# Kernel optimization log

Hardware: AMD Instinct MI355X
Metric: run time of the kernel (lower is better)

The kernel has to match this reference:

```python
import jax, jax.numpy as jnp
import numpy as np

N_NODES = 100000
N_EDGES = 1600000
IN_CH = 128
HID = 64
OUT_CH = 16
N_GRAPHS = 512
NEG_SLOPE = 0.2


def setup_inputs() -> dict:
    key = jax.random.key(0)
    ks = jax.random.split(key, 24)
    x = jax.random.normal(ks[0], (N_NODES, IN_CH), dtype=jnp.float32)
    edge_index = jax.random.randint(ks[1], (2, N_EDGES), 0, N_NODES, dtype=jnp.int64)
    batch = jnp.sort(jax.random.randint(ks[2], (N_NODES,), 0, N_GRAPHS, dtype=jnp.int64))
    s = 0.05
    p = {
        'W_l1': jax.random.normal(ks[3], (IN_CH, HID)) * s,
        'b_l1': jnp.zeros((HID,), jnp.float32),
        'W_r1': jax.random.normal(ks[4], (IN_CH, HID)) * s,
        'b_r1': jnp.zeros((HID,), jnp.float32),
        'att1': jax.random.normal(ks[5], (HID,)) * s,
        'bias1': jnp.zeros((HID,), jnp.float32),
        'W_l2': jax.random.normal(ks[6], (HID, HID)) * s,
        'b_l2': jnp.zeros((HID,), jnp.float32),
        'W_r2': jax.random.normal(ks[7], (HID, HID)) * s,
        'b_r2': jnp.zeros((HID,), jnp.float32),
        'att2': jax.random.normal(ks[8], (HID,)) * s,
        'bias2': jnp.zeros((HID,), jnp.float32),
        'W_fc1': jax.random.normal(ks[9], (HID, HID)) * s,
        'b_fc1': jnp.zeros((HID,), jnp.float32),
        'gamma': jnp.ones((HID,), jnp.float32),
        'beta': jnp.zeros((HID,), jnp.float32),
        'W_fc2': jax.random.normal(ks[10], (HID, OUT_CH)) * s,
        'b_fc2': jnp.zeros((OUT_CH,), jnp.float32),
    }
    return dict(x=x, edge_index=edge_index, batch=batch, **p)


def _gatv2_layer(x, src, dst, Wl, bl, Wr, br, att, bias):
    # GATv2Conv (heads=1): x_l = lin_l(x), x_r = lin_r(x)
    xl = x @ Wl + bl              # [N, H] source transform
    xr = x @ Wr + br              # [N, H] target transform
    # per-edge score: att . LeakyReLU(x_l[j] + x_r[i])
    h = xl[src] + xr[dst]         # [E, H]
    h = jnp.where(h >= 0, h, NEG_SLOPE * h)
    e = h @ att                   # [E]
    # scatter-softmax over incoming edges of each target node
    m = jax.ops.segment_max(e, dst, num_segments=N_NODES)
    a = jnp.exp(e - m[dst])
    z = jax.ops.segment_sum(a, dst, num_segments=N_NODES)
    alpha = a / z[dst]            # every node has a self-loop -> z > 0
    out = jax.ops.segment_sum(alpha[:, None] * xl[src], dst, num_segments=N_NODES)
    return out + bias


def reference(x, edge_index, batch, W_l1, b_l1, W_r1, b_r1, att1, bias1,
              W_l2, b_l2, W_r2, b_r2, att2, bias2,
              W_fc1, b_fc1, gamma, beta, W_fc2, b_fc2):
    loop = jnp.arange(N_NODES, dtype=edge_index.dtype)
    src = jnp.concatenate([edge_index[0], loop])  # add_self_loops=True
    dst = jnp.concatenate([edge_index[1], loop])
    h = _gatv2_layer(x, src, dst, W_l1, b_l1, W_r1, b_r1, att1, bias1)
    h = jax.nn.relu(h)
    h = _gatv2_layer(h, src, dst, W_l2, b_l2, W_r2, b_r2, att2, bias2)
    # global mean pool over graphs
    sums = jax.ops.segment_sum(h, batch, num_segments=N_GRAPHS)
    cnt = jax.ops.segment_sum(jnp.ones((N_NODES,), h.dtype), batch, num_segments=N_GRAPHS)
    g = sums / jnp.clip(cnt, 1.0)[:, None]        # [G, H]
    # MLP head: Linear -> BatchNorm1d (training-mode batch stats) -> ReLU -> Linear
    y = g @ W_fc1 + b_fc1
    mu = jnp.mean(y, axis=0)
    var = jnp.var(y, axis=0)
    y = gamma * (y - mu) * jax.lax.rsqrt(var + 1e-5) + beta
    y = jax.nn.relu(y)
    y = y @ W_fc2 + b_fc2
    return jax.nn.log_softmax(y, axis=1)
```

## Files before the change

### kernel.cpp

```cpp
#include <hip/hip_runtime.h>

#define N_NODES 100000
#define N_EDGES 1600000
#define IN_CH 128
#define HID 64
#define OUT_CH 16
#define N_GRAPHS 512
#define NEG_SLOPE 0.2f

#define MAX_DEG 64

#define GEMM1_BLOCKS ((N_NODES + 127) / 128)
#define DEG_EPT 8
#define DEG_BLOCKS ((N_EDGES + 256 * DEG_EPT - 1) / (256 * DEG_EPT))
#define FUSED_BLOCKS (GEMM1_BLOCKS + DEG_BLOCKS)

#define NEG_BIG (-1e30f)
#define LDSP 132

__device__ __forceinline__ unsigned int f2bf_pack(float lo, float hi) {
  unsigned int ul = __float_as_uint(lo);
  unsigned int uh = __float_as_uint(hi);
  ul = (ul + 0x7FFFu + ((ul >> 16) & 1u)) >> 16;
  uh = (uh + 0x7FFFu + ((uh >> 16) & 1u)) >> 16;
  return ul | (uh << 16);
}
__device__ __forceinline__ float bf2f(unsigned short b) {
  return __uint_as_float(((unsigned int)b) << 16);
}


__global__ __launch_bounds__(256) void k_fused_gemm1_scatter(
    const float* __restrict__ x,
    const float* __restrict__ Wl, const float* __restrict__ bl,
    const float* __restrict__ Wr, const float* __restrict__ br,
    unsigned short* __restrict__ xlb, unsigned short* __restrict__ xrb,
    const int* __restrict__ src, const int* __restrict__ dst,
    int* __restrict__ deg, int* __restrict__ adjP) {
  constexpr int K = IN_CH;
  constexpr int KC = 16;
  constexpr int NCH = K / KC;
  __shared__ float xs[KC][LDSP];
  __shared__ float ws[KC][LDSP];

  int b = blockIdx.x;
  if (b & 1) {
    int db = b >> 1;
    int base = (db * 256 + threadIdx.x) * DEG_EPT;
    if (base + DEG_EPT <= N_EDGES) {
      int4 d4a = *(const int4*)&dst[base];
      int4 d4b = *(const int4*)&dst[base + 4];
      int4 s4a = *(const int4*)&src[base];
      int4 s4b = *(const int4*)&src[base + 4];
      int sl;
      sl = atomicAdd(&deg[d4a.x], 1); if (sl < MAX_DEG) adjP[d4a.x * MAX_DEG + sl] = s4a.x;
      sl = atomicAdd(&deg[d4a.y], 1); if (sl < MAX_DEG) adjP[d4a.y * MAX_DEG + sl] = s4a.y;
      sl = atomicAdd(&deg[d4a.z], 1); if (sl < MAX_DEG) adjP[d4a.z * MAX_DEG + sl] = s4a.z;
      sl = atomicAdd(&deg[d4a.w], 1); if (sl < MAX_DEG) adjP[d4a.w * MAX_DEG + sl] = s4a.w;
      sl = atomicAdd(&deg[d4b.x], 1); if (sl < MAX_DEG) adjP[d4b.x * MAX_DEG + sl] = s4b.x;
      sl = atomicAdd(&deg[d4b.y], 1); if (sl < MAX_DEG) adjP[d4b.y * MAX_DEG + sl] = s4b.y;
      sl = atomicAdd(&deg[d4b.z], 1); if (sl < MAX_DEG) adjP[d4b.z * MAX_DEG + sl] = s4b.z;
      sl = atomicAdd(&deg[d4b.w], 1); if (sl < MAX_DEG) adjP[d4b.w * MAX_DEG + sl] = s4b.w;
    } else {
      for (int e = base; e < N_EDGES; e++) {
        int d = dst[e];
        int sl = atomicAdd(&deg[d], 1);
        if (sl < MAX_DEG) adjP[d * MAX_DEG + sl] = src[e];
      }
    }
    return;
  }

  int tid = threadIdx.x;
  int tx = tid & 15;
  int ty = tid >> 4;
  int nb = (b >> 1) * 128;

  float acc[8][8];
  #pragma unroll
  for (int i = 0; i < 8; i++)
    #pragma unroll
    for (int j = 0; j < 8; j++) acc[i][j] = 0.f;

  for (int c = 0; c < NCH; c++) {
    int kc = c * KC;
    if (c) __syncthreads();
    #pragma unroll
    for (int j = 0; j < 2; j++) {
      int idx = tid + 256 * j;
      int node = idx >> 2, q = idx & 3;
      int gn = nb + node;
      float4 v = make_float4(0.f, 0.f, 0.f, 0.f);
      if (gn < N_NODES) v = *(const float4*)&x[(size_t)gn * K + kc + q * 4];
      xs[q * 4 + 0][node] = v.x;
      xs[q * 4 + 1][node] = v.y;
      xs[q * 4 + 2][node] = v.z;
      xs[q * 4 + 3][node] = v.w;
    }
    #pragma unroll
    for (int j = 0; j < 2; j++) {
      int idx = tid + 256 * j;
      int k = idx >> 5, cc = idx & 31;
      float4 v;
      if (cc < 16) v = *(const float4*)&Wl[(size_t)(kc + k) * 64 + cc * 4];
      else         v = *(const float4*)&Wr[(size_t)(kc + k) * 64 + (cc - 16) * 4];
      *(float4*)&ws[k][cc * 4] = v;
    }
    __syncthreads();

    #pragma unroll 4
    for (int k = 0; k < KC; k++) {
      float4 a0 = *(const float4*)&xs[k][ty * 8];
      float4 a1 = *(const float4*)&xs[k][ty * 8 + 4];
      float4 b0 = *(const float4*)&ws[k][tx * 8];
      float4 b1 = *(const float4*)&ws[k][tx * 8 + 4];
      float av[8] = {a0.x, a0.y, a0.z, a0.w, a1.x, a1.y, a1.z, a1.w};
      float bv[8] = {b0.x, b0.y, b0.z, b0.w, b1.x, b1.y, b1.z, b1.w};
      #pragma unroll
      for (int i = 0; i < 8; i++)
        #pragma unroll
        for (int j = 0; j < 8; j++)
          acc[i][j] = fmaf(av[i], bv[j], acc[i][j]);
    }
  }

  int f0 = tx * 8;
  float bb[8];
  #pragma unroll
  for (int j = 0; j < 8; j++)
    bb[j] = (f0 < 64) ? bl[f0 + j] : br[f0 - 64 + j];
  unsigned short* outp = (f0 < 64) ? xlb : xrb;
  int fo = (f0 < 64) ? f0 : f0 - 64;
  #pragma unroll
  for (int i = 0; i < 8; i++) {
    int node = nb + ty * 8 + i;
    if (node < N_NODES) {
      int4 o;
      o.x = (int)f2bf_pack(acc[i][0] + bb[0], acc[i][1] + bb[1]);
      o.y = (int)f2bf_pack(acc[i][2] + bb[2], acc[i][3] + bb[3]);
      o.z = (int)f2bf_pack(acc[i][4] + bb[4], acc[i][5] + bb[5]);
      o.w = (int)f2bf_pack(acc[i][6] + bb[6], acc[i][7] + bb[7]);
      *(int4*)&outp[(size_t)node * 64 + fo] = o;
    }
  }
}


template <int K>
__global__ __launch_bounds__(256) void k_dual_gemm(
    const float* __restrict__ x,
    const float* __restrict__ Wl, const float* __restrict__ bl,
    const float* __restrict__ Wr, const float* __restrict__ br,
    unsigned short* __restrict__ xlb, unsigned short* __restrict__ xrb) {
  constexpr int KC = 32;
  constexpr int NCH = K / KC;
  __shared__ float xs[KC][LDSP];
  __shared__ float ws[KC][LDSP];

  int tid = threadIdx.x;
  int tx = tid & 15;
  int ty = tid >> 4;
  int nb = blockIdx.x * 128;

  float acc[8][8];
  #pragma unroll
  for (int i = 0; i < 8; i++)
    #pragma unroll
    for (int j = 0; j < 8; j++) acc[i][j] = 0.f;

  for (int c = 0; c < NCH; c++) {
    int kc = c * KC;
    if (c) __syncthreads();
    #pragma unroll
    for (int j = 0; j < 4; j++) {
      int idx = tid + 256 * j;
      int node = idx >> 3, q = idx & 7;
      int gn = nb + node;
      float4 v = make_float4(0.f, 0.f, 0.f, 0.f);
      if (gn < N_NODES) v = *(const float4*)&x[(size_t)gn * K + kc + q * 4];
      xs[q * 4 + 0][node] = v.x;
      xs[q * 4 + 1][node] = v.y;
      xs[q * 4 + 2][node] = v.z;
      xs[q * 4 + 3][node] = v.w;
    }
    #pragma unroll
    for (int j = 0; j < 4; j++) {
      int idx = tid + 256 * j;
      int k = idx >> 5, cc = idx & 31;
      float4 v;
      if (cc < 16) v = *(const float4*)&Wl[(size_t)(kc + k) * 64 + cc * 4];
      else         v = *(const float4*)&Wr[(size_t)(kc + k) * 64 + (cc - 16) * 4];
      *(float4*)&ws[k][cc * 4] = v;
    }
    __syncthreads();

    #pragma unroll 4
    for (int k = 0; k < KC; k++) {
      float4 a0 = *(const float4*)&xs[k][ty * 8];
      float4 a1 = *(const float4*)&xs[k][ty * 8 + 4];
      float4 b0 = *(const float4*)&ws[k][tx * 8];
      float4 b1 = *(const float4*)&ws[k][tx * 8 + 4];
      float av[8] = {a0.x, a0.y, a0.z, a0.w, a1.x, a1.y, a1.z, a1.w};
      float bv[8] = {b0.x, b0.y, b0.z, b0.w, b1.x, b1.y, b1.z, b1.w};
      #pragma unroll
      for (int i = 0; i < 8; i++)
        #pragma unroll
        for (int j = 0; j < 8; j++)
          acc[i][j] = fmaf(av[i], bv[j], acc[i][j]);
    }
  }

  int f0 = tx * 8;
  float bb[8];
  #pragma unroll
  for (int j = 0; j < 8; j++)
    bb[j] = (f0 < 64) ? bl[f0 + j] : br[f0 - 64 + j];
  unsigned short* outp = (f0 < 64) ? xlb : xrb;
  int fo = (f0 < 64) ? f0 : f0 - 64;
  #pragma unroll
  for (int i = 0; i < 8; i++) {
    int node = nb + ty * 8 + i;
    if (node < N_NODES) {
      int4 o;
      o.x = (int)f2bf_pack(acc[i][0] + bb[0], acc[i][1] + bb[1]);
      o.y = (int)f2bf_pack(acc[i][2] + bb[2], acc[i][3] + bb[3]);
      o.z = (int)f2bf_pack(acc[i][4] + bb[4], acc[i][5] + bb[5]);
      o.w = (int)f2bf_pack(acc[i][6] + bb[6], acc[i][7] + bb[7]);
      *(int4*)&outp[(size_t)node * 64 + fo] = o;
    }
  }
}


__global__ __launch_bounds__(256) void k_gat(
    const unsigned short* __restrict__ xlb, const unsigned short* __restrict__ xrb,
    const float* __restrict__ att, const float* __restrict__ bias,
    const int* __restrict__ deg, const int* __restrict__ adjP,
    float* __restrict__ out, int do_relu) {
  int wid = (blockIdx.x * 256 + threadIdx.x) >> 6;
  int lane = threadIdx.x & 63;
  if (wid >= N_NODES) return;
  int fg = lane & 15;
  int sub = lane >> 4;

  int degv = deg[wid];
  degv = (degv < MAX_DEG) ? degv : MAX_DEG;
  int L = degv + 1;

  int eidx = wid;
  if (lane < degv) eidx = adjP[(size_t)wid * MAX_DEG + lane];

  ushort4 xrr = *(const ushort4*)&xrb[(size_t)wid * 64 + fg * 4];
  float4 xr4;
  xr4.x = bf2f(xrr.x); xr4.y = bf2f(xrr.y); xr4.z = bf2f(xrr.z); xr4.w = bf2f(xrr.w);
  float4 att4 = *(const float4*)&att[fg * 4];

  float m = NEG_BIG, z = 0.f;
  float4 acc = make_float4(0.f, 0.f, 0.f, 0.f);

  for (int p0 = 0; p0 < L; p0 += 8) {
    int q0 = p0 + sub * 2;
    int q1 = q0 + 1;
    bool act0 = (q0 < L);
    bool act1 = (q1 < L);
    int idx0 = q0 - 1;
    int idx1 = q1 - 1;
    int sj0 = __shfl(eidx, idx0 & 63, 64);
    int sj1 = __shfl(eidx, idx1 & 63, 64);
    int j0 = (q0 == 0) ? wid : sj0;
    int j1 = sj1;
    ushort4 raw0 = make_ushort4(0, 0, 0, 0);
    ushort4 raw1 = make_ushort4(0, 0, 0, 0);
    if (act0) raw0 = *(const ushort4*)&xlb[(size_t)j0 * 64 + fg * 4];
    if (act1) raw1 = *(const ushort4*)&xlb[(size_t)j1 * 64 + fg * 4];
    float4 v0, v1;
    v0.x = bf2f(raw0.x); v0.y = bf2f(raw0.y); v0.z = bf2f(raw0.z); v0.w = bf2f(raw0.w);
    v1.x = bf2f(raw1.x); v1.y = bf2f(raw1.y); v1.z = bf2f(raw1.z); v1.w = bf2f(raw1.w);

    float ax, ay, az, aw;
    ax = v0.x + xr4.x; ax = (ax >= 0.f) ? ax : NEG_SLOPE * ax;
    ay = v0.y + xr4.y; ay = (ay >= 0.f) ? ay : NEG_SLOPE * ay;
    az = v0.z + xr4.z; az = (az >= 0.f) ? az : NEG_SLOPE * az;
    aw = v0.w + xr4.w; aw = (aw >= 0.f) ? aw : NEG_SLOPE * aw;
    float s0 = fmaf(ax, att4.x, fmaf(ay, att4.y, fmaf(az, att4.z, aw * att4.w)));
    ax = v1.x + xr4.x; ax = (ax >= 0.f) ? ax : NEG_SLOPE * ax;
    ay = v1.y + xr4.y; ay = (ay >= 0.f) ? ay : NEG_SLOPE * ay;
    az = v1.z + xr4.z; az = (az >= 0.f) ? az : NEG_SLOPE * az;
    aw = v1.w + xr4.w; aw = (aw >= 0.f) ? aw : NEG_SLOPE * aw;
    float s1 = fmaf(ax, att4.x, fmaf(ay, att4.y, fmaf(az, att4.z, aw * att4.w)));
    #pragma unroll
    for (int o = 1; o <= 8; o <<= 1) {
      s0 += __shfl_xor(s0, o, 64);
      s1 += __shfl_xor(s1, o, 64);
    }
    float e0 = act0 ? s0 : NEG_BIG;
    float e1 = act1 ? s1 : NEG_BIG;

    float nm = fmaxf(m, fmaxf(e0, e1));
    float sc = __expf(m - nm);
    float w0 = __expf(e0 - nm);
    float w1 = __expf(e1 - nm);
    z = fmaf(z, sc, w0 + w1);
    acc.x = fmaf(acc.x, sc, fmaf(w0, v0.x, w1 * v1.x));
    acc.y = fmaf(acc.y, sc, fmaf(w0, v0.y, w1 * v1.y));
    acc.z = fmaf(acc.z, sc, fmaf(w0, v0.z, w1 * v1.z));
    acc.w = fmaf(acc.w, sc, fmaf(w0, v0.w, w1 * v1.w));
    m = nm;
  }

  #pragma unroll
  for (int o = 16; o <= 32; o <<= 1) {
    float m2 = __shfl_xor(m, o, 64);
    float z2 = __shfl_xor(z, o, 64);
    float a0 = __shfl_xor(acc.x, o, 64);
    float a1 = __shfl_xor(acc.y, o, 64);
    float a2 = __shfl_xor(acc.z, o, 64);
    float a3 = __shfl_xor(acc.w, o, 64);
    float nm = fmaxf(m, m2);
    float s1 = __expf(m - nm);
    float s2 = __expf(m2 - nm);
    z = z * s1 + z2 * s2;
    acc.x = acc.x * s1 + a0 * s2;
    acc.y = acc.y * s1 + a1 * s2;
    acc.z = acc.z * s1 + a2 * s2;
    acc.w = acc.w * s1 + a3 * s2;
    m = nm;
  }

  if (sub == 0) {
    float4 b4 = *(const float4*)&bias[fg * 4];
    float inv = 1.f / z;
    float4 r;
    r.x = acc.x * inv + b4.x;
    r.y = acc.y * inv + b4.y;
    r.z = acc.z * inv + b4.z;
    r.w = acc.w * inv + b4.w;
    if (do_relu) {
      r.x = fmaxf(r.x, 0.f); r.y = fmaxf(r.y, 0.f);
      r.z = fmaxf(r.z, 0.f); r.w = fmaxf(r.w, 0.f);
    }
    *(float4*)&out[(size_t)wid * 64 + fg * 4] = r;
  }
}


__device__ __forceinline__ int lower_bound_batch(const int* __restrict__ b, int key) {
  int lo = 0, hi = N_NODES;
  while (lo < hi) {
    int mid = (lo + hi) >> 1;
    if (b[mid] < key) lo = mid + 1; else hi = mid;
  }
  return lo;
}

__global__ void k_pool(const float* __restrict__ h, const int* __restrict__ batch,
                       float* __restrict__ gmean) {
  __shared__ int s_range[2];
  __shared__ float red[256];
  int g = blockIdx.x, t = threadIdx.x;
  if (t == 0) s_range[0] = lower_bound_batch(batch, g);
  if (t == 1) s_range[1] = lower_bound_batch(batch, g + 1);
  __syncthreads();
  int lo = s_range[0], hi = s_range[1];
  int f = t & 63, sub = t >> 6;
  float acc = 0.f;
  for (int n = lo + sub; n < hi; n += 4) acc += h[n * 64 + f];
  red[t] = acc;
  __syncthreads();
  if (sub == 0) {
    float s = red[f] + red[64 + f] + red[128 + f] + red[192 + f];
    int cnt = hi - lo;
    if (cnt < 1) cnt = 1;
    gmean[g * 64 + f] = s / (float)cnt;
  }
}


__global__ void k_head1(const float* __restrict__ gmean, const float* __restrict__ W,
                        const float* __restrict__ b, float* __restrict__ y) {
  int idx = blockIdx.x * 256 + threadIdx.x;
  if (idx >= N_GRAPHS * 64) return;
  int gi = idx >> 6, f = idx & 63;
  float acc = b[f];
  #pragma unroll 8
  for (int k = 0; k < 64; k++) acc = fmaf(gmean[gi * 64 + k], W[k * 64 + f], acc);
  y[idx] = acc;
}

__global__ void k_bnstats(const float* __restrict__ y, float* __restrict__ mu,
                          float* __restrict__ rstd) {
  __shared__ float red_s[256], red_ss[256];
  int t = threadIdx.x;
  int f = t & 63, grp = t >> 6;
  float s = 0.f, ss = 0.f;
  for (int g = grp; g < N_GRAPHS; g += 4) {
    float v = y[g * 64 + f];
    s += v;
    ss += v * v;
  }
  red_s[t] = s;
  red_ss[t] = ss;
  __syncthreads();
  if (t < 64) {
    s = red_s[t] + red_s[64 + t] + red_s[128 + t] + red_s[192 + t];
    ss = red_ss[t] + red_ss[64 + t] + red_ss[128 + t] + red_ss[192 + t];
    float m = s / (float)N_GRAPHS;
    float var = ss / (float)N_GRAPHS - m * m;
    mu[t] = m;
    rstd[t] = rsqrtf(var + 1e-5f);
  }
}

__global__ void k_head2(const float* __restrict__ y, const float* __restrict__ gamma,
                        const float* __restrict__ beta, const float* __restrict__ mu,
                        const float* __restrict__ rstd, const float* __restrict__ W2,
                        const float* __restrict__ b2, float* __restrict__ out) {
  int idx = blockIdx.x * 256 + threadIdx.x;
  if (idx >= N_GRAPHS * OUT_CH) return;
  int gi = idx >> 4, o = idx & 15;
  float acc = b2[o];
  #pragma unroll
  for (int k = 0; k < 64; k++) {
    float v = y[gi * 64 + k];
    v = gamma[k] * (v - mu[k]) * rstd[k] + beta[k];
    v = fmaxf(v, 0.f);
    acc = fmaf(v, W2[k * OUT_CH + o], acc);
  }
  float mx = acc;
  #pragma unroll
  for (int w = 8; w > 0; w >>= 1) mx = fmaxf(mx, __shfl_xor(mx, w, 16));
  float ex = __expf(acc - mx);
  float s = ex;
  #pragma unroll
  for (int w = 8; w > 0; w >>= 1) s += __shfl_xor(s, w, 16);
  out[idx] = acc - mx - __logf(s);
}


extern "C" void kernel_launch(void* const* d_in, const int* in_sizes, int n_in,
                              void* d_out, int out_size, void* d_ws, size_t ws_size,
                              hipStream_t stream) {
  const float* x      = (const float*)d_in[0];
  const int*   edge   = (const int*)d_in[1];
  const int*   batch  = (const int*)d_in[2];
  const float* W_l1   = (const float*)d_in[3];
  const float* b_l1   = (const float*)d_in[4];
  const float* W_r1   = (const float*)d_in[5];
  const float* b_r1   = (const float*)d_in[6];
  const float* att1   = (const float*)d_in[7];
  const float* bias1  = (const float*)d_in[8];
  const float* W_l2   = (const float*)d_in[9];
  const float* b_l2   = (const float*)d_in[10];
  const float* W_r2   = (const float*)d_in[11];
  const float* b_r2   = (const float*)d_in[12];
  const float* att2   = (const float*)d_in[13];
  const float* bias2  = (const float*)d_in[14];
  const float* W_fc1  = (const float*)d_in[15];
  const float* b_fc1  = (const float*)d_in[16];
  const float* gamma  = (const float*)d_in[17];
  const float* beta   = (const float*)d_in[18];
  const float* W_fc2  = (const float*)d_in[19];
  const float* b_fc2  = (const float*)d_in[20];

  const int* src = edge;
  const int* dst = edge + N_EDGES;

  char* ws = (char*)d_ws;
  size_t off = 0;
  auto alloc = [&](size_t bytes) -> void* {
    off = (off + 255) & ~(size_t)255;
    void* p = ws + off;
    off += bytes;
    return p;
  };
  int* deg      = (int*)alloc((size_t)N_NODES * 4);
  int* adjP     = (int*)alloc((size_t)N_NODES * MAX_DEG * 4);
  unsigned short* xlb = (unsigned short*)alloc((size_t)N_NODES * HID * 2);
  unsigned short* xrb = (unsigned short*)alloc((size_t)N_NODES * HID * 2);
  float* h      = (float*)alloc((size_t)N_NODES * HID * 4);
  float* gmean  = (float*)alloc((size_t)N_GRAPHS * HID * 4);
  float* y      = (float*)alloc((size_t)N_GRAPHS * HID * 4);
  float* mu     = (float*)alloc(64 * 4);
  float* rstd   = (float*)alloc(64 * 4);

  hipMemsetAsync(deg, 0, (size_t)N_NODES * 4, stream);

  k_fused_gemm1_scatter<<<FUSED_BLOCKS, 256, 0, stream>>>(
      x, W_l1, b_l1, W_r1, b_r1, xlb, xrb, src, dst, deg, adjP);

  k_gat<<<(N_NODES + 3) / 4, 256, 0, stream>>>(xlb, xrb, att1, bias1, deg, adjP, h, 1);
  k_dual_gemm<HID><<<(N_NODES + 127) / 128, 256, 0, stream>>>(h, W_l2, b_l2, W_r2, b_r2, xlb, xrb);
  k_gat<<<(N_NODES + 3) / 4, 256, 0, stream>>>(xlb, xrb, att2, bias2, deg, adjP, h, 0);

  k_pool<<<N_GRAPHS, 256, 0, stream>>>(h, batch, gmean);
  k_head1<<<(N_GRAPHS * 64 + 255) / 256, 256, 0, stream>>>(gmean, W_fc1, b_fc1, y);
  k_bnstats<<<1, 256, 0, stream>>>(y, mu, rstd);
  k_head2<<<(N_GRAPHS * OUT_CH + 255) / 256, 256, 0, stream>>>(y, gamma, beta, mu, rstd,
                                                               W_fc2, b_fc2, (float*)d_out);
}
```

Baseline: 436.4 us.

## Fuse layer-2 dual linear transform into first GAT aggregation epilogue

Result: slower. 469.8 us (+7.7%).

```diff
diff --git a/kernel.cpp b/kernel.cpp
--- a/kernel.cpp
+++ b/kernel.cpp
@@ -24,6 +24,11 @@
   ul = (ul + 0x7FFFu + ((ul >> 16) & 1u)) >> 16;
   uh = (uh + 0x7FFFu + ((uh >> 16) & 1u)) >> 16;
   return ul | (uh << 16);
+}
+__device__ __forceinline__ unsigned short f2bf(float v) {
+  unsigned int u = __float_as_uint(v);
+  u = (u + 0x7FFFu + ((u >> 16) & 1u)) >> 16;
+  return (unsigned short)u;
 }
 __device__ __forceinline__ float bf2f(unsigned short b) {
   return __uint_as_float(((unsigned int)b) << 16);
@@ -146,97 +151,14 @@
 }
 
 
-template <int K>
-__global__ __launch_bounds__(256) void k_dual_gemm(
-    const float* __restrict__ x,
-    const float* __restrict__ Wl, const float* __restrict__ bl,
-    const float* __restrict__ Wr, const float* __restrict__ br,
-    unsigned short* __restrict__ xlb, unsigned short* __restrict__ xrb) {
-  constexpr int KC = 32;
-  constexpr int NCH = K / KC;
-  __shared__ float xs[KC][LDSP];
-  __shared__ float ws[KC][LDSP];
-
-  int tid = threadIdx.x;
-  int tx = tid & 15;
-  int ty = tid >> 4;
-  int nb = blockIdx.x * 128;
-
-  float acc[8][8];
-  #pragma unroll
-  for (int i = 0; i < 8; i++)
-    #pragma unroll
-    for (int j = 0; j < 8; j++) acc[i][j] = 0.f;
-
-  for (int c = 0; c < NCH; c++) {
-    int kc = c * KC;
-    if (c) __syncthreads();
-    #pragma unroll
-    for (int j = 0; j < 4; j++) {
-      int idx = tid + 256 * j;
-      int node = idx >> 3, q = idx & 7;
-      int gn = nb + node;
-      float4 v = make_float4(0.f, 0.f, 0.f, 0.f);
-      if (gn < N_NODES) v = *(const float4*)&x[(size_t)gn * K + kc + q * 4];
-      xs[q * 4 + 0][node] = v.x;
-      xs[q * 4 + 1][node] = v.y;
-      xs[q * 4 + 2][node] = v.z;
-      xs[q * 4 + 3][node] = v.w;
-    }
-    #pragma unroll
-    for (int j = 0; j < 4; j++) {
-      int idx = tid + 256 * j;
-      int k = idx >> 5, cc = idx & 31;
-      float4 v;
-      if (cc < 16) v = *(const float4*)&Wl[(size_t)(kc + k) * 64 + cc * 4];
-      else         v = *(const float4*)&Wr[(size_t)(kc + k) * 64 + (cc - 16) * 4];
-      *(float4*)&ws[k][cc * 4] = v;
-    }
-    __syncthreads();
-
-    #pragma unroll 4
-    for (int k = 0; k < KC; k++) {
-      float4 a0 = *(const float4*)&xs[k][ty * 8];
-      float4 a1 = *(const float4*)&xs[k][ty * 8 + 4];
-      float4 b0 = *(const float4*)&ws[k][tx * 8];
-      float4 b1 = *(const float4*)&ws[k][tx * 8 + 4];
-      float av[8] = {a0.x, a0.y, a0.z, a0.w, a1.x, a1.y, a1.z, a1.w};
-      float bv[8] = {b0.x, b0.y, b0.z, b0.w, b1.x, b1.y, b1.z, b1.w};
-      #pragma unroll
-      for (int i = 0; i < 8; i++)
-        #pragma unroll
-        for (int j = 0; j < 8; j++)
-          acc[i][j] = fmaf(av[i], bv[j], acc[i][j]);
-    }
-  }
-
-  int f0 = tx * 8;
-  float bb[8];
-  #pragma unroll
-  for (int j = 0; j < 8; j++)
-    bb[j] = (f0 < 64) ? bl[f0 + j] : br[f0 - 64 + j];
-  unsigned short* outp = (f0 < 64) ? xlb : xrb;
-  int fo = (f0 < 64) ? f0 : f0 - 64;
-  #pragma unroll
-  for (int i = 0; i < 8; i++) {
-    int node = nb + ty * 8 + i;
-    if (node < N_NODES) {
-      int4 o;
-      o.x = (int)f2bf_pack(acc[i][0] + bb[0], acc[i][1] + bb[1]);
-      o.y = (int)f2bf_pack(acc[i][2] + bb[2], acc[i][3] + bb[3]);
-      o.z = (int)f2bf_pack(acc[i][4] + bb[4], acc[i][5] + bb[5]);
-      o.w = (int)f2bf_pack(acc[i][6] + bb[6], acc[i][7] + bb[7]);
-      *(int4*)&outp[(size_t)node * 64 + fo] = o;
-    }
-  }
-}
-
-
 __global__ __launch_bounds__(256) void k_gat(
     const unsigned short* __restrict__ xlb, const unsigned short* __restrict__ xrb,
     const float* __restrict__ att, const float* __restrict__ bias,
     const int* __restrict__ deg, const int* __restrict__ adjP,
-    float* __restrict__ out, int do_relu) {
+    const float* __restrict__ Wl2, const float* __restrict__ bl2,
+    const float* __restrict__ Wr2, const float* __restrict__ br2,
+    unsigned short* __restrict__ xlb_out, unsigned short* __restrict__ xrb_out,
+    float* __restrict__ hout, int mode) {
   int wid = (blockIdx.x * 256 + threadIdx.x) >> 6;
   int lane = threadIdx.x & 63;
   if (wid >= N_NODES) return;
@@ -327,19 +249,32 @@
     m = nm;
   }
 
-  if (sub == 0) {
-    float4 b4 = *(const float4*)&bias[fg * 4];
-    float inv = 1.f / z;
-    float4 r;
-    r.x = acc.x * inv + b4.x;
-    r.y = acc.y * inv + b4.y;
-    r.z = acc.z * inv + b4.z;
-    r.w = acc.w * inv + b4.w;
-    if (do_relu) {
-      r.x = fmaxf(r.x, 0.f); r.y = fmaxf(r.y, 0.f);
-      r.z = fmaxf(r.z, 0.f); r.w = fmaxf(r.w, 0.f);
-    }
-    *(float4*)&out[(size_t)wid * 64 + fg * 4] = r;
+  float inv = 1.f / z;
+  float4 b4 = *(const float4*)&bias[fg * 4];
+  float4 r;
+  r.x = acc.x * inv + b4.x;
+  r.y = acc.y * inv + b4.y;
+  r.z = acc.z * inv + b4.z;
+  r.w = acc.w * inv + b4.w;
+
+  if (mode) {
+    r.x = fmaxf(r.x, 0.f); r.y = fmaxf(r.y, 0.f);
+    r.z = fmaxf(r.z, 0.f); r.w = fmaxf(r.w, 0.f);
+    float y0 = 0.f, y1 = 0.f;
+    #pragma unroll
+    for (int k = 0; k < 64; k++) {
+      float comp = ((k & 3) == 0) ? r.x : ((k & 3) == 1) ? r.y
+                 : ((k & 3) == 2) ? r.z : r.w;
+      float hk = __shfl(comp, k >> 2, 64);
+      y0 = fmaf(hk, Wl2[k * 64 + lane], y0);
+      y1 = fmaf(hk, Wr2[k * 64 + lane], y1);
+    }
+    y0 += bl2[lane];
+    y1 += br2[lane];
+    xlb_out[(size_t)wid * 64 + lane] = f2bf(y0);
+    xrb_out[(size_t)wid * 64 + lane] = f2bf(y1);
+  } else if (sub == 0) {
+    *(float4*)&hout[(size_t)wid * 64 + fg * 4] = r;
   }
 }
 
@@ -483,16 +418,24 @@
   float* mu     = (float*)alloc(64 * 4);
   float* rstd   = (float*)alloc(64 * 4);
 
+  unsigned short* xlb2 = (unsigned short*)h;
+  unsigned short* xrb2 = xlb2 + (size_t)N_NODES * HID;
+  float* h2 = (float*)xlb;
+
   hipMemsetAsync(deg, 0, (size_t)N_NODES * 4, stream);
 
   k_fused_gemm1_scatter<<<FUSED_BLOCKS, 256, 0, stream>>>(
       x, W_l1, b_l1, W_r1, b_r1, xlb, xrb, src, dst, deg, adjP);
 
-  k_gat<<<(N_NODES + 3) / 4, 256, 0, stream>>>(xlb, xrb, att1, bias1, deg, adjP, h, 1);
-  k_dual_gemm<HID><<<(N_NODES + 127) / 128, 256, 0, stream>>>(h, W_l2, b_l2, W_r2, b_r2, xlb, xrb);
-  k_gat<<<(N_NODES + 3) / 4, 256, 0, stream>>>(xlb, xrb, att2, bias2, deg, adjP, h, 0);
-
-  k_pool<<<N_GRAPHS, 256, 0, stream>>>(h, batch, gmean);
+  k_gat<<<(N_NODES + 3) / 4, 256, 0, stream>>>(
+      xlb, xrb, att1, bias1, deg, adjP,
+      W_l2, b_l2, W_r2, b_r2, xlb2, xrb2, (float*)nullptr, 1);
+
+  k_gat<<<(N_NODES + 3) / 4, 256, 0, stream>>>(
+      xlb2, xrb2, att2, bias2, deg, adjP,
+      W_l2, b_l2, W_r2, b_r2, (unsigned short*)nullptr, (unsigned short*)nullptr, h2, 0);
+
+  k_pool<<<N_GRAPHS, 256, 0, stream>>>(h2, batch, gmean);
   k_head1<<<(N_GRAPHS * 64 + 255) / 256, 256, 0, stream>>>(gmean, W_fc1, b_fc1, y);
   k_bnstats<<<1, 256, 0, stream>>>(y, mu, rstd);
   k_head2<<<(N_GRAPHS * OUT_CH + 255) / 256, 256, 0, stream>>>(y, gamma, beta, mu, rstd,
```

## Restructure GAT kernel into two-pass softmax with per-lane edge scoring

Applied to the files above, without the earlier changes.

After: 506.7 us. 16.1% more time.

```diff
diff --git a/kernel.cpp b/kernel.cpp
--- a/kernel.cpp
+++ b/kernel.cpp
@@ -27,6 +27,12 @@
 }
 __device__ __forceinline__ float bf2f(unsigned short b) {
   return __uint_as_float(((unsigned int)b) << 16);
+}
+__device__ __forceinline__ float bfu_lo(int u) {
+  return __uint_as_float(((unsigned int)u) << 16);
+}
+__device__ __forceinline__ float bfu_hi(int u) {
+  return __uint_as_float(((unsigned int)u) & 0xFFFF0000u);
 }
 
 
@@ -240,91 +246,76 @@
   int wid = (blockIdx.x * 256 + threadIdx.x) >> 6;
   int lane = threadIdx.x & 63;
   if (wid >= N_NODES) return;
+
+  int degv = deg[wid];
+  degv = (degv < 63) ? degv : 63;
+  int L = degv + 1;
+
+  int j = wid;
+  if (lane >= 1 && lane <= degv) j = adjP[(size_t)wid * MAX_DEG + (lane - 1)];
+
+  float s0 = 0.f, s1 = 0.f, s2 = 0.f, s3 = 0.f;
+  if (lane < L) {
+    const unsigned short* row = &xlb[(size_t)j * 64];
+    #pragma unroll
+    for (int c = 0; c < 8; c++) {
+      int4 raw = *(const int4*)&row[c * 8];
+      int4 xrr = *(const int4*)&xrb[(size_t)wid * 64 + c * 8];
+      float4 a0 = *(const float4*)&att[c * 8];
+      float4 a1 = *(const float4*)&att[c * 8 + 4];
+      float h;
+      h = bfu_lo(raw.x) + bfu_lo(xrr.x); h = (h >= 0.f) ? h : NEG_SLOPE * h; s0 = fmaf(h, a0.x, s0);
+      h = bfu_hi(raw.x) + bfu_hi(xrr.x); h = (h >= 0.f) ? h : NEG_SLOPE * h; s1 = fmaf(h, a0.y, s1);
+      h = bfu_lo(raw.y) + bfu_lo(xrr.y); h = (h >= 0.f) ? h : NEG_SLOPE * h; s2 = fmaf(h, a0.z, s2);
+      h = bfu_hi(raw.y) + bfu_hi(xrr.y); h = (h >= 0.f) ? h : NEG_SLOPE * h; s3 = fmaf(h, a0.w, s3);
+      h = bfu_lo(raw.z) + bfu_lo(xrr.z); h = (h >= 0.f) ? h : NEG_SLOPE * h; s0 = fmaf(h, a1.x, s0);
+      h = bfu_hi(raw.z) + bfu_hi(xrr.z); h = (h >= 0.f) ? h : NEG_SLOPE * h; s1 = fmaf(h, a1.y, s1);
+      h = bfu_lo(raw.w) + bfu_lo(xrr.w); h = (h >= 0.f) ? h : NEG_SLOPE * h; s2 = fmaf(h, a1.z, s2);
+      h = bfu_hi(raw.w) + bfu_hi(xrr.w); h = (h >= 0.f) ? h : NEG_SLOPE * h; s3 = fmaf(h, a1.w, s3);
+    }
+  }
+  float e = (lane < L) ? ((s0 + s1) + (s2 + s3)) : NEG_BIG;
+
+  float m = e;
+  #pragma unroll
+  for (int o = 1; o < 64; o <<= 1) m = fmaxf(m, __shfl_xor(m, o, 64));
+  float w = __expf(e - m);
+  float z = w;
+  #pragma unroll
+  for (int o = 1; o < 64; o <<= 1) z += __shfl_xor(z, o, 64);
+
   int fg = lane & 15;
   int sub = lane >> 4;
-
-  int degv = deg[wid];
-  degv = (degv < MAX_DEG) ? degv : MAX_DEG;
-  int L = degv + 1;
-
-  int eidx = wid;
-  if (lane < degv) eidx = adjP[(size_t)wid * MAX_DEG + lane];
-
-  ushort4 xrr = *(const ushort4*)&xrb[(size_t)wid * 64 + fg * 4];
-  float4 xr4;
-  xr4.x = bf2f(xrr.x); xr4.y = bf2f(xrr.y); xr4.z = bf2f(xrr.z); xr4.w = bf2f(xrr.w);
-  float4 att4 = *(const float4*)&att[fg * 4];
-
-  float m = NEG_BIG, z = 0.f;
   float4 acc = make_float4(0.f, 0.f, 0.f, 0.f);
-
   for (int p0 = 0; p0 < L; p0 += 8) {
     int q0 = p0 + sub * 2;
     int q1 = q0 + 1;
-    bool act0 = (q0 < L);
-    bool act1 = (q1 < L);
-    int idx0 = q0 - 1;
-    int idx1 = q1 - 1;
-    int sj0 = __shfl(eidx, idx0 & 63, 64);
-    int sj1 = __shfl(eidx, idx1 & 63, 64);
-    int j0 = (q0 == 0) ? wid : sj0;
-    int j1 = sj1;
-    ushort4 raw0 = make_ushort4(0, 0, 0, 0);
-    ushort4 raw1 = make_ushort4(0, 0, 0, 0);
-    if (act0) raw0 = *(const ushort4*)&xlb[(size_t)j0 * 64 + fg * 4];
-    if (act1) raw1 = *(const ushort4*)&xlb[(size_t)j1 * 64 + fg * 4];
-    float4 v0, v1;
-    v0.x = bf2f(raw0.x); v0.y = bf2f(raw0.y); v0.z = bf2f(raw0.z); v0.w = bf2f(raw0.w);
-    v1.x = bf2f(raw1.x); v1.y = bf2f(raw1.y); v1.z = bf2f(raw1.z); v1.w = bf2f(raw1.w);
-
-    float ax, ay, az, aw;
-    ax = v0.x + xr4.x; ax = (ax >= 0.f) ? ax : NEG_SLOPE * ax;
-    ay = v0.y + xr4.y; ay = (ay >= 0.f) ? ay : NEG_SLOPE * ay;
-    az = v0.z + xr4.z; az = (az >= 0.f) ? az : NEG_SLOPE * az;
-    aw = v0.w + xr4.w; aw = (aw >= 0.f) ? aw : NEG_SLOPE * aw;
-    float s0 = fmaf(ax, att4.x, fmaf(ay, att4.y, fmaf(az, att4.z, aw * att4.w)));
-    ax = v1.x + xr4.x; ax = (ax >= 0.f) ? ax : NEG_SLOPE * ax;
-    ay = v1.y + xr4.y; ay = (ay >= 0.f) ? ay : NEG_SLOPE * ay;
-    az = v1.z + xr4.z; az = (az >= 0.f) ? az : NEG_SLOPE * az;
-    aw = v1.w + xr4.w; aw = (aw >= 0.f) ? aw : NEG_SLOPE * aw;
-    float s1 = fmaf(ax, att4.x, fmaf(ay, att4.y, fmaf(az, att4.z, aw * att4.w)));
-    #pragma unroll
-    for (int o = 1; o <= 8; o <<= 1) {
-      s0 += __shfl_xor(s0, o, 64);
-      s1 += __shfl_xor(s1, o, 64);
-    }
-    float e0 = act0 ? s0 : NEG_BIG;
-    float e1 = act1 ? s1 : NEG_BIG;
-
-    float nm = fmaxf(m, fmaxf(e0, e1));
-    float sc = __expf(m - nm);
-    float w0 = __expf(e0 - nm);
-    float w1 = __expf(e1 - nm);
-    z = fmaf(z, sc, w0 + w1);
-    acc.x = fmaf(acc.x, sc, fmaf(w0, v0.x, w1 * v1.x));
-    acc.y = fmaf(acc.y, sc, fmaf(w0, v0.y, w1 * v1.y));
-    acc.z = fmaf(acc.z, sc, fmaf(w0, v0.z, w1 * v1.z));
-    acc.w = fmaf(acc.w, sc, fmaf(w0, v0.w, w1 * v1.w));
-    m = nm;
+    float w0 = __shfl(w, q0 & 63, 64);
+    float w1 = __shfl(w, q1 & 63, 64);
+    int j0 = __shfl(j, q0 & 63, 64);
+    int j1 = __shfl(j, q1 & 63, 64);
+    if (q0 < L) {
+      ushort4 r = *(const ushort4*)&xlb[(size_t)j0 * 64 + fg * 4];
+      acc.x = fmaf(w0, bf2f(r.x), acc.x);
+      acc.y = fmaf(w0, bf2f(r.y), acc.y);
+      acc.z = fmaf(w0, bf2f(r.z), acc.z);
+      acc.w = fmaf(w0, bf2f(r.w), acc.w);
+    }
+    if (q1 < L) {
+      ushort4 r = *(const ushort4*)&xlb[(size_t)j1 * 64 + fg * 4];
+      acc.x = fmaf(w1, bf2f(r.x), acc.x);
+      acc.y = fmaf(w1, bf2f(r.y), acc.y);
+      acc.z = fmaf(w1, bf2f(r.z), acc.z);
+      acc.w = fmaf(w1, bf2f(r.w), acc.w);
+    }
   }
 
   #pragma unroll
   for (int o = 16; o <= 32; o <<= 1) {
-    float m2 = __shfl_xor(m, o, 64);
-    float z2 = __shfl_xor(z, o, 64);
-    float a0 = __shfl_xor(acc.x, o, 64);
-    float a1 = __shfl_xor(acc.y, o, 64);
-    float a2 = __shfl_xor(acc.z, o, 64);
-    float a3 = __shfl_xor(acc.w, o, 64);
-    float nm = fmaxf(m, m2);
-    float s1 = __expf(m - nm);
-    float s2 = __expf(m2 - nm);
-    z = z * s1 + z2 * s2;
-    acc.x = acc.x * s1 + a0 * s2;
-    acc.y = acc.y * s1 + a1 * s2;
-    acc.z = acc.z * s1 + a2 * s2;
-    acc.w = acc.w * s1 + a3 * s2;
-    m = nm;
+    acc.x += __shfl_xor(acc.x, o, 64);
+    acc.y += __shfl_xor(acc.y, o, 64);
+    acc.z += __shfl_xor(acc.z, o, 64);
+    acc.w += __shfl_xor(acc.w, o, 64);
   }
 
   if (sub == 0) {
```
